# Performance work log

Measured on AMD Instinct MI355X. Metric: run time of the kernel, lower is better.

The kernel has to match this reference:

```python
import jax, jax.numpy as jnp
import numpy as np

B, T, N_EMBD, H, D_HEAD = 4, 2048, 1024, 16, 64

def setup_inputs() -> dict:
    key = jax.random.key(0)
    ks = jax.random.split(key, 6)
    s_in = N_EMBD ** -0.5
    x = jax.random.normal(ks[0], (B, T, N_EMBD), dtype=jnp.float32)
    # per-head Linear(n_embd, d_head, bias=False) weights, stacked: [H, n_embd, d_head]
    Wq = jax.random.normal(ks[1], (H, N_EMBD, D_HEAD), dtype=jnp.float32) * s_in
    Wk = jax.random.normal(ks[2], (H, N_EMBD, D_HEAD), dtype=jnp.float32) * s_in
    Wv = jax.random.normal(ks[3], (H, N_EMBD, D_HEAD), dtype=jnp.float32) * s_in
    # proj: Linear(H*d_head, n_embd) with bias
    Wp = jax.random.normal(ks[4], (H * D_HEAD, N_EMBD), dtype=jnp.float32) * ((H * D_HEAD) ** -0.5)
    bp = jax.random.normal(ks[5], (N_EMBD,), dtype=jnp.float32) * 0.01
    return {"x": x, "Wq": Wq, "Wk": Wk, "Wv": Wv, "Wp": Wp, "bp": bp}

def reference(x, Wq, Wk, Wv, Wp, bp):
    # per-head projections: [B, H, T, d_head]
    q = jnp.einsum('btc,hcd->bhtd', x, Wq)
    k = jnp.einsum('btc,hcd->bhtd', x, Wk)
    v = jnp.einsum('btc,hcd->bhtd', x, Wv)
    scale = q.shape[-1] ** -0.5
    # full (ring-accumulated across P=1 step) non-causal attention
    scores = jnp.einsum('bhtd,bhsd->bhts', q, k) * scale  # [B,H,T,T]
    p = jax.nn.softmax(scores, axis=-1)
    o = jnp.einsum('bhts,bhsd->bhtd', p, v)               # [B,H,T,d]
    o = o.transpose(0, 2, 1, 3).reshape(x.shape[0], x.shape[1], -1)  # [B,T,H*d]
    out = o @ Wp + bp  # output projection (dropout in eval mode = identity)
    return out
```

## Files before the change

kernel.cpp:

```cpp
#include <hip/hip_runtime.h>
#include <hip/hip_bf16.h>

#define T_SEQ 2048
#define NE    1024
#define NH    16
#define DH    64
#define MROWS 8192
#define QKV_N 3072

typedef __attribute__((ext_vector_type(8))) short bf16x8;
typedef __attribute__((ext_vector_type(4))) float f32x4;

__device__ __forceinline__ ushort f2b(float f) {
  uint u = __builtin_bit_cast(uint, f);
  return (ushort)((u + 0x7fffu + ((u >> 16) & 1u)) >> 16);
}
__device__ __forceinline__ float b2f(ushort u) {
  uint v = ((uint)u) << 16;
  return __builtin_bit_cast(float, v);
}

__device__ __forceinline__ void gload_lds16(const ushort* g, ushort* l) {
  __builtin_amdgcn_global_load_lds(
      (const __attribute__((address_space(1))) void*)g,
      (__attribute__((address_space(3))) void*)l, 16, 0, 0);
}

__global__ void cvt_x_kernel(const float* __restrict__ x, ushort* __restrict__ xb) {
  int i = blockIdx.x * blockDim.x + threadIdx.x;
  float4 v = reinterpret_cast<const float4*>(x)[i];
  ushort4 o;
  o.x = f2b(v.x); o.y = f2b(v.y); o.z = f2b(v.z); o.w = f2b(v.w);
  reinterpret_cast<ushort4*>(xb)[i] = o;
}

__global__ void wtrans_head(const float* __restrict__ W, ushort* __restrict__ outT, int rowoff) {
  int h = blockIdx.y;
  int c0 = blockIdx.x * 64;
  __shared__ float t[64][65];
  int a = threadIdx.x & 63, i0 = (threadIdx.x >> 6) * 16;
  const float* base = W + (size_t)h * NE * DH;
#pragma unroll
  for (int j = 0; j < 16; ++j)
    t[i0 + j][a] = base[(size_t)(c0 + i0 + j) * DH + a];
  __syncthreads();
#pragma unroll
  for (int j = 0; j < 16; ++j) {
    int d = i0 + j;
    outT[(size_t)(rowoff + h * DH + d) * NE + c0 + a] = f2b(t[a][d]);
  }
}

__global__ void wtrans_sq(const float* __restrict__ W, ushort* __restrict__ outT) {
  int k0 = blockIdx.x * 64, n0 = blockIdx.y * 64;
  __shared__ float t[64][65];
  int a = threadIdx.x & 63, i0 = (threadIdx.x >> 6) * 16;
#pragma unroll
  for (int j = 0; j < 16; ++j)
    t[i0 + j][a] = W[(size_t)(k0 + i0 + j) * NE + n0 + a];
  __syncthreads();
#pragma unroll
  for (int j = 0; j < 16; ++j) {
    int n = i0 + j;
    outT[(size_t)(n0 + n) * NE + k0 + a] = f2b(t[a][n]);
  }
}

template <int OUTF32>
__global__ __launch_bounds__(256, 2) void gemm_bt(
    const ushort* __restrict__ A, const ushort* __restrict__ Bt,
    void* __restrict__ Cout, const float* __restrict__ bias,
    int M, int N, int K) {
  __shared__ alignas(16) ushort Als[128 * 32];
  __shared__ alignas(16) ushort Bls[128 * 32];
  const int tid = threadIdx.x;
  const int lane = tid & 63, w = tid >> 6;
  const int wr = w >> 1, wc = w & 1;
  const int c = lane & 15, g = lane >> 4;
  const int arow0 = blockIdx.x * 128, brow0 = blockIdx.y * 128;
  const int srow = lane >> 2, scol = (lane & 3) * 8;

  f32x4 acc[4][4];
  f32x4 zero = {0.f, 0.f, 0.f, 0.f};
#pragma unroll
  for (int i = 0; i < 4; ++i)
#pragma unroll
    for (int j = 0; j < 4; ++j) acc[i][j] = zero;

  for (int k0 = 0; k0 < K; k0 += 32) {
#pragma unroll
    for (int cc = 0; cc < 2; ++cc) {
      int ch = w * 2 + cc;
      const ushort* ga = A + (size_t)(arow0 + ch * 16 + srow) * K + k0 + scol;
      gload_lds16(ga, &Als[ch * 512]);
      const ushort* gb = Bt + (size_t)(brow0 + ch * 16 + srow) * K + k0 + scol;
      gload_lds16(gb, &Bls[ch * 512]);
    }
    __syncthreads();

    bf16x8 af[4], bfr[4];
#pragma unroll
    for (int t4 = 0; t4 < 4; ++t4) {
      af[t4]  = *(const bf16x8*)&Als[(wr * 64 + t4 * 16 + c) * 32 + g * 8];
      bfr[t4] = *(const bf16x8*)&Bls[(wc * 64 + t4 * 16 + c) * 32 + g * 8];
    }
#pragma unroll
    for (int i = 0; i < 4; ++i)
#pragma unroll
      for (int j = 0; j < 4; ++j)
        acc[i][j] = __builtin_amdgcn_mfma_f32_16x16x32_bf16(af[i], bfr[j], acc[i][j], 0, 0, 0);
    __syncthreads();
  }

#pragma unroll
  for (int i = 0; i < 4; ++i)
#pragma unroll
    for (int j = 0; j < 4; ++j)
#pragma unroll
      for (int r = 0; r < 4; ++r) {
        int row = arow0 + wr * 64 + i * 16 + g * 4 + r;
        int col = brow0 + wc * 64 + j * 16 + c;
        float v = acc[i][j][r];
        if constexpr (OUTF32) {
          ((float*)Cout)[(size_t)row * N + col] = v + bias[col];
        } else {
          ((ushort*)Cout)[(size_t)row * N + col] = f2b(v);
        }
      }
}

__global__ __launch_bounds__(256, 2) void attn_kern(
    const ushort* __restrict__ qkv, ushort* __restrict__ obuf) {
  const int flat = blockIdx.x;
  const int logical = (flat & 7) * 256 + (flat >> 3);
  const int qt = logical & 31, bh = logical >> 5;
  const int b = bh >> 4, h = bh & 15;
  const int lane = threadIdx.x & 63, w = threadIdx.x >> 6;
  const int c = lane & 15, g = lane >> 4;
  const size_t row0 = (size_t)b * T_SEQ;
  const int qc = h * 64, kc = 1024 + h * 64, vc = 2048 + h * 64;
  const int tid = threadIdx.x;

  __shared__ alignas(16) ushort Kls[2][64 * 64];
  __shared__ alignas(16) ushort Vt[2][64 * 64];
  __shared__ alignas(16) ushort Pls[4][16 * 64];

  const float SCL = 0.125f * 1.44269504f;
  bf16x8 aq[2];
  {
    const size_t qrow = row0 + qt * 64 + w * 16 + c;
    aq[0] = *(const bf16x8*)&qkv[qrow * QKV_N + qc + g * 8];
    aq[1] = *(const bf16x8*)&qkv[qrow * QKV_N + qc + 32 + g * 8];
  }

  const int kj0 = tid >> 3, kdc = (tid & 7) * 8;
  const int kj1 = (tid + 256) >> 3;
  const int vd0 = (tid & 31) * 2, vs0 = (tid >> 5) * 8;

  float l_part[4] = {0.f, 0.f, 0.f, 0.f};
  f32x4 zero = {0.f, 0.f, 0.f, 0.f};
  f32x4 oacc[4];
#pragma unroll
  for (int dt = 0; dt < 4; ++dt) oacc[dt] = zero;

  {
    bf16x8 k0 = *(const bf16x8*)&qkv[(row0 + kj0) * QKV_N + kc + kdc];
    bf16x8 k1 = *(const bf16x8*)&qkv[(row0 + kj1) * QKV_N + kc + kdc];
    *(bf16x8*)&Kls[0][(kj0 * 64 + kdc) ^ ((kj0 & 7) << 3)] = k0;
    *(bf16x8*)&Kls[0][(kj1 * 64 + kdc) ^ ((kj1 & 7) << 3)] = k1;
    uint vr[8];
#pragma unroll
    for (int i = 0; i < 8; ++i)
      vr[i] = *(const uint*)&qkv[(row0 + vs0 + i) * QKV_N + vc + vd0];
    bf16x8 lo, hi;
#pragma unroll
    for (int i = 0; i < 8; ++i) { lo[i] = (short)(vr[i] & 0xffff); hi[i] = (short)(vr[i] >> 16); }
    *(bf16x8*)&Vt[0][(vd0 * 64 + vs0) ^ ((vd0 & 7) << 3)] = lo;
    *(bf16x8*)&Vt[0][((vd0 + 1) * 64 + vs0) ^ (((vd0 + 1) & 7) << 3)] = hi;
  }
  __syncthreads();

  int cur = 0;
  for (int tile = 0; tile < T_SEQ / 64; ++tile) {
    bf16x8 k0, k1, vlo, vhi;
    if (tile + 1 < T_SEQ / 64) {
      const size_t kv = (size_t)(tile + 1) * 64;
      k0 = *(const bf16x8*)&qkv[(row0 + kv + kj0) * QKV_N + kc + kdc];
      k1 = *(const bf16x8*)&qkv[(row0 + kv + kj1) * QKV_N + kc + kdc];
      uint vr[8];
#pragma unroll
      for (int i = 0; i < 8; ++i)
        vr[i] = *(const uint*)&qkv[(row0 + kv + vs0 + i) * QKV_N + vc + vd0];
#pragma unroll
      for (int i = 0; i < 8; ++i) { vlo[i] = (short)(vr[i] & 0xffff); vhi[i] = (short)(vr[i] >> 16); }
    }

    f32x4 sa[4];
#pragma unroll
    for (int jt = 0; jt < 4; ++jt) sa[jt] = zero;
#pragma unroll
    for (int ks = 0; ks < 2; ++ks)
#pragma unroll
      for (int jt = 0; jt < 4; ++jt) {
        int j = jt * 16 + c;
        bf16x8 bk = *(const bf16x8*)&Kls[cur][(j * 64 + ks * 32 + g * 8) ^ ((j & 7) << 3)];
        sa[jt] = __builtin_amdgcn_mfma_f32_16x16x32_bf16(aq[ks], bk, sa[jt], 0, 0, 0);
      }

    float pp[4][4];
#pragma unroll
    for (int jt = 0; jt < 4; ++jt)
#pragma unroll
      for (int r = 0; r < 4; ++r) pp[jt][r] = exp2f(sa[jt][r] * SCL);
#pragma unroll
    for (int r = 0; r < 4; ++r)
      l_part[r] += (pp[0][r] + pp[1][r]) + (pp[2][r] + pp[3][r]);

#pragma unroll
    for (int jt = 0; jt < 4; ++jt)
#pragma unroll
      for (int r = 0; r < 4; ++r) {
        int i = g * 4 + r, s = jt * 16 + c;
        Pls[w][(i * 64 + s) ^ ((i & 7) << 3)] = f2b(pp[jt][r]);
      }

#pragma unroll
    for (int ks = 0; ks < 2; ++ks) {
      bf16x8 ap = *(const bf16x8*)&Pls[w][(c * 64 + ks * 32 + g * 8) ^ ((c & 7) << 3)];
#pragma unroll
      for (int dt = 0; dt < 4; ++dt) {
        int d = dt * 16 + c;
        bf16x8 bv = *(const bf16x8*)&Vt[cur][(d * 64 + ks * 32 + g * 8) ^ ((d & 7) << 3)];
        oacc[dt] = __builtin_amdgcn_mfma_f32_16x16x32_bf16(ap, bv, oacc[dt], 0, 0, 0);
      }
    }

    if (tile + 1 < T_SEQ / 64) {
      int nb = cur ^ 1;
      *(bf16x8*)&Kls[nb][(kj0 * 64 + kdc) ^ ((kj0 & 7) << 3)] = k0;
      *(bf16x8*)&Kls[nb][(kj1 * 64 + kdc) ^ ((kj1 & 7) << 3)] = k1;
      *(bf16x8*)&Vt[nb][(vd0 * 64 + vs0) ^ ((vd0 & 7) << 3)] = vlo;
      *(bf16x8*)&Vt[nb][((vd0 + 1) * 64 + vs0) ^ (((vd0 + 1) & 7) << 3)] = vhi;
    }
    __syncthreads();
    cur ^= 1;
  }

#pragma unroll
  for (int r = 0; r < 4; ++r) {
    float L = l_part[r];
#pragma unroll
    for (int mask = 1; mask < 16; mask <<= 1) L += __shfl_xor(L, mask);
    float rinv = 1.0f / L;
#pragma unroll
    for (int dt = 0; dt < 4; ++dt) {
      int R = qt * 64 + w * 16 + g * 4 + r;
      int d = dt * 16 + c;
      obuf[(row0 + R) * (size_t)NE + h * 64 + d] = f2b(oacc[dt][r] * rinv);
    }
  }
}

extern "C" void kernel_launch(void* const* d_in, const int* in_sizes, int n_in,
                              void* d_out, int out_size, void* d_ws, size_t ws_size,
                              hipStream_t stream) {
  const float* x  = (const float*)d_in[0];
  const float* Wq = (const float*)d_in[1];
  const float* Wk = (const float*)d_in[2];
  const float* Wv = (const float*)d_in[3];
  const float* Wp = (const float*)d_in[4];
  const float* bp = (const float*)d_in[5];
  float* out = (float*)d_out;

  char* ws = (char*)d_ws;
  ushort* xb    = (ushort*)(ws + 0);
  ushort* WcatT = (ushort*)(ws + 16777216);
  ushort* WpT   = (ushort*)(ws + 23068672);
  ushort* qkv   = (ushort*)(ws + 25165824);
  ushort* obuf  = (ushort*)(ws + 75497472);

  cvt_x_kernel<<<dim3(8192), dim3(256), 0, stream>>>(x, xb);
  wtrans_head<<<dim3(16, 16), dim3(256), 0, stream>>>(Wq, WcatT, 0);
  wtrans_head<<<dim3(16, 16), dim3(256), 0, stream>>>(Wk, WcatT, 1024);
  wtrans_head<<<dim3(16, 16), dim3(256), 0, stream>>>(Wv, WcatT, 2048);
  wtrans_sq<<<dim3(16, 16), dim3(256), 0, stream>>>(Wp, WpT);

  gemm_bt<0><<<dim3(MROWS / 128, QKV_N / 128), dim3(256), 0, stream>>>(
      xb, WcatT, (void*)qkv, nullptr, MROWS, QKV_N, NE);

  attn_kern<<<dim3(2048), dim3(256), 0, stream>>>(qkv, obuf);

  gemm_bt<1><<<dim3(MROWS / 128, NE / 128), dim3(256), 0, stream>>>(
      obuf, WpT, (void*)out, bp, MROWS, NE, NE);
}
```

Measured before the change: 345.4 us.

## Load K tiles directly to LDS, use raw v_exp, raise attention occupancy

K tiles in the attention kernel are now fetched with global_load_lds straight into shared memory. The XOR swizzle moves onto the global source column so the LDS layout stays the same, and the register staging and later LDS stores for K are dropped. exp2f is replaced with the raw v_exp_f32 instruction, the bf16 conversion uses the HIP intrinsic, and launch bounds ask for 4 blocks per CU instead of 2. The intent is lower register pressure and fewer VALU/LDS instructions, at the cost of possible register spills and of the async LDS write needing correct waits before the barrier.

```diff
diff --git a/kernel.cpp b/kernel.cpp
--- a/kernel.cpp
+++ b/kernel.cpp
@@ -7,17 +7,17 @@
 #define DH    64
 #define MROWS 8192
 #define QKV_N 3072
+#define NT    (T_SEQ / 64)
 
 typedef __attribute__((ext_vector_type(8))) short bf16x8;
 typedef __attribute__((ext_vector_type(4))) float f32x4;
 
 __device__ __forceinline__ ushort f2b(float f) {
-  uint u = __builtin_bit_cast(uint, f);
-  return (ushort)((u + 0x7fffu + ((u >> 16) & 1u)) >> 16);
-}
-__device__ __forceinline__ float b2f(ushort u) {
-  uint v = ((uint)u) << 16;
-  return __builtin_bit_cast(float, v);
+  __hip_bfloat16 h = __float2bfloat16(f);
+  return *reinterpret_cast<ushort*>(&h);
+}
+__device__ __forceinline__ float fast_exp2(float x) {
+  float r; asm("v_exp_f32 %0, %1" : "=v"(r) : "v"(x)); return r;
 }
 
 __device__ __forceinline__ void gload_lds16(const ushort* g, ushort* l) {
@@ -129,7 +129,7 @@
       }
 }
 
-__global__ __launch_bounds__(256, 2) void attn_kern(
+__global__ __launch_bounds__(256, 4) void attn_kern(
     const ushort* __restrict__ qkv, ushort* __restrict__ obuf) {
   const int flat = blockIdx.x;
   const int logical = (flat & 7) * 256 + (flat >> 3);
@@ -153,8 +153,10 @@
     aq[1] = *(const bf16x8*)&qkv[qrow * QKV_N + qc + 32 + g * 8];
   }
 
-  const int kj0 = tid >> 3, kdc = (tid & 7) * 8;
-  const int kj1 = (tid + 256) >> 3;
+  const int kq0 = (w * 2 + 0) * 64 + lane;
+  const int kq1 = (w * 2 + 1) * 64 + lane;
+  const int kj0 = kq0 >> 3, kcc0 = ((kq0 & 7) ^ (kj0 & 7)) * 8;
+  const int kj1 = kq1 >> 3, kcc1 = ((kq1 & 7) ^ (kj1 & 7)) * 8;
   const int vd0 = (tid & 31) * 2, vs0 = (tid >> 5) * 8;
 
   float l_part[4] = {0.f, 0.f, 0.f, 0.f};
@@ -164,10 +166,8 @@
   for (int dt = 0; dt < 4; ++dt) oacc[dt] = zero;
 
   {
-    bf16x8 k0 = *(const bf16x8*)&qkv[(row0 + kj0) * QKV_N + kc + kdc];
-    bf16x8 k1 = *(const bf16x8*)&qkv[(row0 + kj1) * QKV_N + kc + kdc];
-    *(bf16x8*)&Kls[0][(kj0 * 64 + kdc) ^ ((kj0 & 7) << 3)] = k0;
-    *(bf16x8*)&Kls[0][(kj1 * 64 + kdc) ^ ((kj1 & 7) << 3)] = k1;
+    gload_lds16(&qkv[(row0 + kj0) * QKV_N + kc + kcc0], &Kls[0][(w * 2 + 0) * 512]);
+    gload_lds16(&qkv[(row0 + kj1) * QKV_N + kc + kcc1], &Kls[0][(w * 2 + 1) * 512]);
     uint vr[8];
 #pragma unroll
     for (int i = 0; i < 8; ++i)
@@ -181,12 +181,13 @@
   __syncthreads();
 
   int cur = 0;
-  for (int tile = 0; tile < T_SEQ / 64; ++tile) {
-    bf16x8 k0, k1, vlo, vhi;
-    if (tile + 1 < T_SEQ / 64) {
+  for (int tile = 0; tile < NT; ++tile) {
+    const int nb = cur ^ 1;
+    bf16x8 vlo, vhi;
+    if (tile + 1 < NT) {
       const size_t kv = (size_t)(tile + 1) * 64;
-      k0 = *(const bf16x8*)&qkv[(row0 + kv + kj0) * QKV_N + kc + kdc];
-      k1 = *(const bf16x8*)&qkv[(row0 + kv + kj1) * QKV_N + kc + kdc];
+      gload_lds16(&qkv[(row0 + kv + kj0) * QKV_N + kc + kcc0], &Kls[nb][(w * 2 + 0) * 512]);
+      gload_lds16(&qkv[(row0 + kv + kj1) * QKV_N + kc + kcc1], &Kls[nb][(w * 2 + 1) * 512]);
       uint vr[8];
 #pragma unroll
       for (int i = 0; i < 8; ++i)
@@ -211,7 +212,7 @@
 #pragma unroll
     for (int jt = 0; jt < 4; ++jt)
 #pragma unroll
-      for (int r = 0; r < 4; ++r) pp[jt][r] = exp2f(sa[jt][r] * SCL);
+      for (int r = 0; r < 4; ++r) pp[jt][r] = fast_exp2(sa[jt][r] * SCL);
 #pragma unroll
     for (int r = 0; r < 4; ++r)
       l_part[r] += (pp[0][r] + pp[1][r]) + (pp[2][r] + pp[3][r]);
@@ -235,10 +236,7 @@
       }
     }
 
-    if (tile + 1 < T_SEQ / 64) {
-      int nb = cur ^ 1;
-      *(bf16x8*)&Kls[nb][(kj0 * 64 + kdc) ^ ((kj0 & 7) << 3)] = k0;
-      *(bf16x8*)&Kls[nb][(kj1 * 64 + kdc) ^ ((kj1 & 7) << 3)] = k1;
+    if (tile + 1 < NT) {
       *(bf16x8*)&Vt[nb][(vd0 * 64 + vs0) ^ ((vd0 & 7) << 3)] = vlo;
       *(bf16x8*)&Vt[nb][((vd0 + 1) * 64 + vs0) ^ (((vd0 + 1) & 7) << 3)] = vhi;
     }
```

After: 313.5 us. 1.1x faster.
